# Optimization experiments

Measured on AMD Instinct MI355X. Metric: run time of the kernel, lower is better.

## Reference

```python
import jax, jax.numpy as jnp
import numpy as np
from jax import lax

B, CIN, H, W = 64, 16, 256, 256
COUT, K = 64, 3

def setup_inputs() -> dict:
    key = jax.random.key(0)
    k1, k2, k3 = jax.random.split(key, 3)
    x = jax.random.normal(k1, (B, CIN, H, W), dtype=jnp.float32)
    # PyTorch Conv2d default init scale ~ 1/sqrt(fan_in)
    fan_in = CIN * K * K
    conv_weight = jax.random.normal(k2, (COUT, CIN, K, K), dtype=jnp.float32) / np.sqrt(fan_in)
    conv_bias = jax.random.normal(k3, (COUT,), dtype=jnp.float32) / np.sqrt(fan_in)
    return {"x": x, "conv_weight": conv_weight, "conv_bias": conv_bias}

def reference(x, conv_weight, conv_bias):
    # conv2d, stride=1, padding=0 (VALID), dilation=1, groups=1
    y = lax.conv_general_dilated(
        x, conv_weight,
        window_strides=(1, 1), padding="VALID",
        dimension_numbers=("NCHW", "OIHW", "NCHW"))
    y = y + conv_bias[None, :, None, None]
    # min over channel dim, keepdim
    y = jnp.min(y, axis=1, keepdims=True)  # [B,1,H',W']
    # double tanh
    return jnp.tanh(jnp.tanh(y))
```

## Files before the change

### kernel.cpp

```cpp
#include <hip/hip_runtime.h>
#include <hip/hip_bf16.h>

#define BATCH 64
#define CIN   16
#define H     256
#define W     256
#define HW    (H*W)
#define COUT  64
#define HO    254
#define WO    254

#define TS     16
#define TIN    18
#define CELL   24
#define NTY    8
#define NITEMS (4*TIN*TIN)
#define IPT    6

typedef short  bf16x8 __attribute__((ext_vector_type(8)));
typedef float  f32x16 __attribute__((ext_vector_type(16)));

static __device__ __forceinline__ unsigned short bfbits(float f) {
    __hip_bfloat16 h = __float2bfloat16(f);
    return *(unsigned short*)&h;
}

static __device__ __forceinline__ bf16x8 ld_frag(const ushort* p) {
    union { uint4 u; bf16x8 b; } cv;
    cv.u = *(const uint4*)p;
    return cv.b;
}

static __device__ __forceinline__ float fast_tanh(float x) {
    x = fminf(fmaxf(x, -15.f), 15.f);
    float e = __expf(2.f * x);
    return (e - 1.f) * __builtin_amdgcn_rcpf(e + 1.f);
}

__global__ void repack_w(const float* __restrict__ w, ushort* __restrict__ wpk) {
    int i = blockIdx.x * 256 + threadIdx.x;
    if (i < 9 * COUT * CIN) {
        int ci   = i & 15;
        int cout = (i >> 4) & 63;
        int tap  = i >> 10;
        wpk[i] = bfbits(w[(cout * CIN + ci) * 9 + tap]);
    }
}

__global__ __launch_bounds__(256, 2)
void conv_min_tanh_strip(const float* __restrict__ x,
                         const float* __restrict__ bias,
                         const ushort* __restrict__ wpk,
                         float* __restrict__ out) {
    __shared__ __align__(16) ushort xsm[2][TIN * TIN * CELL];

    const int bid    = blockIdx.x;
    const int L      = (bid & 7) * 256 + (bid >> 3);
    const int b      = L >> 5;
    const int rr     = L & 31;
    const int yb0    = (rr >> 4) * (NTY * TS);
    const int x0     = (rr & 15) * TS;

    const int tid  = threadIdx.x;
    const int lane = tid & 63;
    const int wv   = tid >> 6;
    const int l31  = lane & 31;
    const int hi   = lane >> 5;

    const float* xb0 = x + (size_t)b * (CIN * HW);
    const float* xb1 = xb0 + HW;
    const float* xb2 = xb0 + 2 * HW;
    const float* xb3 = xb0 + 3 * HW;

    bf16x8 wf[9][2];
    #pragma unroll
    for (int tap = 0; tap < 9; ++tap)
        #pragma unroll
        for (int m = 0; m < 2; ++m)
            wf[tap][m] = ld_frag(wpk + tap * 1024 + (m * 32 + l31) * 16 + hi * 8);

    float bini[2][16];
    #pragma unroll
    for (int m = 0; m < 2; ++m)
        #pragma unroll
        for (int r = 0; r < 16; ++r)
            bini[m][r] = bias[m * 32 + (r & 3) + 8 * (r >> 2) + 4 * hi];

    int c0[IPT], dyv[IPT], lo[IPT];
    #pragma unroll
    for (int k = 0; k < IPT; ++k) {
        int it = tid + k * 256;
        int dx = it % TIN;
        int t2 = it / TIN;
        int dy = t2 % TIN;
        int cg = t2 / TIN;
        c0[k]  = cg * 4 * HW + min(x0 + dx, W - 1);
        dyv[k] = dy;
        lo[k]  = (dy * TIN + dx) * CELL + cg * 4;
    }

    const int py_b = wv * 4 + (l31 >> 4);
    const int pxc  = l31 & 15;
    const int cb0  = ((py_b + 0) * TIN + pxc) * CELL + hi * 8;
    const int cb1  = ((py_b + 2) * TIN + pxc) * CELL + hi * 8;

    float fx[IPT][4];

    auto stage_load = [&](int ybase) {
        #pragma unroll
        for (int k = 0; k < IPT; ++k) {
            if (k < 5 || tid < NITEMS - 5 * 256) {
                int gy  = min(ybase + dyv[k], H - 1);
                int idx = c0[k] + (gy << 8);
                fx[k][0] = xb0[idx];
                fx[k][1] = xb1[idx];
                fx[k][2] = xb2[idx];
                fx[k][3] = xb3[idx];
            }
        }
    };
    auto stage_write = [&](int buf) {
        #pragma unroll
        for (int k = 0; k < IPT; ++k) {
            if (k < 5 || tid < NITEMS - 5 * 256) {
                ushort4 v;
                v.x = bfbits(fx[k][0]);
                v.y = bfbits(fx[k][1]);
                v.z = bfbits(fx[k][2]);
                v.w = bfbits(fx[k][3]);
                *(ushort4*)&xsm[buf][lo[k]] = v;
            }
        }
    };

    stage_load(yb0);
    stage_write(0);
    __syncthreads();

    for (int t = 0; t < NTY; ++t) {
        const int cur = t & 1;

        if (t + 1 < NTY) stage_load(yb0 + (t + 1) * TS);

        f32x16 acc[2][2];
        #pragma unroll
        for (int m = 0; m < 2; ++m)
            #pragma unroll
            for (int r = 0; r < 16; ++r) {
                acc[m][0][r] = bini[m][r];
                acc[m][1][r] = bini[m][r];
            }

        const ushort* xt = &xsm[cur][0];
        #pragma unroll
        for (int tap = 0; tap < 9; ++tap) {
            const int kh = tap / 3, kw = tap - 3 * kh;
            const int toff = (kh * TIN + kw) * CELL;
            bf16x8 p0 = ld_frag(xt + cb0 + toff);
            bf16x8 p1 = ld_frag(xt + cb1 + toff);
            acc[0][0] = __builtin_amdgcn_mfma_f32_32x32x16_bf16(wf[tap][0], p0, acc[0][0], 0, 0, 0);
            acc[0][1] = __builtin_amdgcn_mfma_f32_32x32x16_bf16(wf[tap][0], p1, acc[0][1], 0, 0, 0);
            acc[1][0] = __builtin_amdgcn_mfma_f32_32x32x16_bf16(wf[tap][1], p0, acc[1][0], 0, 0, 0);
            acc[1][1] = __builtin_amdgcn_mfma_f32_32x32x16_bf16(wf[tap][1], p1, acc[1][1], 0, 0, 0);
        }

        float res[2];
        #pragma unroll
        for (int n = 0; n < 2; ++n) {
            float v[16];
            #pragma unroll
            for (int r = 0; r < 16; ++r)
                v[r] = fminf(acc[0][n][r], acc[1][n][r]);
            #pragma unroll
            for (int s = 8; s >= 1; s >>= 1)
                #pragma unroll
                for (int r = 0; r < s; ++r)
                    v[r] = fminf(v[r], v[r + s]);
            res[n] = fminf(v[0], __shfl_xor(v[0], 32, 64));
        }
        float val = hi ? res[1] : res[0];
        int px_lin = wv * 64 + lane;
        int oy = yb0 + t * TS + (px_lin >> 4);
        int ox = x0 + (px_lin & 15);
        if (oy < HO && ox < WO)
            out[((size_t)b * HO + oy) * WO + ox] = fast_tanh(fast_tanh(val));

        if (t + 1 < NTY) stage_write(cur ^ 1);
        __syncthreads();
    }
}

extern "C" void kernel_launch(void* const* d_in, const int* in_sizes, int n_in,
                              void* d_out, int out_size, void* d_ws, size_t ws_size,
                              hipStream_t stream) {
    const float* x    = (const float*)d_in[0];
    const float* w    = (const float*)d_in[1];
    const float* bias = (const float*)d_in[2];
    float* out        = (float*)d_out;
    ushort* wpk       = (ushort*)d_ws;

    hipLaunchKernelGGL(repack_w, dim3(36), dim3(256), 0, stream, w, wpk);
    hipLaunchKernelGGL(conv_min_tanh_strip, dim3(2048), dim3(256), 0, stream,
                       x, bias, wpk, out);
}
```

Measured before the change: 106.9 us.

## Deepen input prefetch to two tiles and fold bias into an extra MFMA

Input loading now runs two tiles ahead, ping-ponging between two register sets. This hides more global-load latency behind the MFMA work, and the LDS staging write moves before the epilogue. The bias is packed as a tenth weight tap and multiplied by a constant 'one' fragment, which frees the 32 bias-init registers. The cost is an extra MFMA per accumulator per tile, plus one more bf16 rounding of the bias. The barrier is lowered to a bare lgkmcnt wait plus s_barrier, and MFMA priority is raised with s_setprio. Register pressure rises from the second prefetch buffer and the extra weight fragments.

```diff
diff --git a/kernel.cpp b/kernel.cpp
--- a/kernel.cpp
+++ b/kernel.cpp
@@ -37,29 +37,34 @@
     return (e - 1.f) * __builtin_amdgcn_rcpf(e + 1.f);
 }
 
-__global__ void repack_w(const float* __restrict__ w, ushort* __restrict__ wpk) {
+__global__ void repack_w(const float* __restrict__ w, const float* __restrict__ bias,
+                         ushort* __restrict__ wpk) {
     int i = blockIdx.x * 256 + threadIdx.x;
     if (i < 9 * COUT * CIN) {
         int ci   = i & 15;
         int cout = (i >> 4) & 63;
         int tap  = i >> 10;
         wpk[i] = bfbits(w[(cout * CIN + ci) * 9 + tap]);
+    } else if (i < 10 * COUT * CIN) {
+        int j    = i - 9 * COUT * CIN;
+        int ci   = j & 15;
+        int cout = j >> 4;
+        wpk[i] = (ci == 0) ? bfbits(bias[cout]) : (ushort)0;
     }
 }
 
 __global__ __launch_bounds__(256, 2)
 void conv_min_tanh_strip(const float* __restrict__ x,
-                         const float* __restrict__ bias,
                          const ushort* __restrict__ wpk,
                          float* __restrict__ out) {
     __shared__ __align__(16) ushort xsm[2][TIN * TIN * CELL];
 
-    const int bid    = blockIdx.x;
-    const int L      = (bid & 7) * 256 + (bid >> 3);
-    const int b      = L >> 5;
-    const int rr     = L & 31;
-    const int yb0    = (rr >> 4) * (NTY * TS);
-    const int x0     = (rr & 15) * TS;
+    const int bid = blockIdx.x;
+    const int L   = (bid & 7) * 256 + (bid >> 3);
+    const int b   = L >> 5;
+    const int rr  = L & 31;
+    const int yb0 = (rr >> 4) * (NTY * TS);
+    const int x0  = (rr & 15) * TS;
 
     const int tid  = threadIdx.x;
     const int lane = tid & 63;
@@ -67,24 +72,22 @@
     const int l31  = lane & 31;
     const int hi   = lane >> 5;
 
-    const float* xb0 = x + (size_t)b * (CIN * HW);
-    const float* xb1 = xb0 + HW;
-    const float* xb2 = xb0 + 2 * HW;
-    const float* xb3 = xb0 + 3 * HW;
-
-    bf16x8 wf[9][2];
+    const float* xp0 = x + (size_t)b * (CIN * HW);
+    const float* xp1 = xp0 + HW;
+    const float* xp2 = xp0 + 2 * HW;
+    const float* xp3 = xp0 + 3 * HW;
+
+    bf16x8 wf[10][2];
     #pragma unroll
-    for (int tap = 0; tap < 9; ++tap)
+    for (int tap = 0; tap < 10; ++tap)
         #pragma unroll
         for (int m = 0; m < 2; ++m)
             wf[tap][m] = ld_frag(wpk + tap * 1024 + (m * 32 + l31) * 16 + hi * 8);
 
-    float bini[2][16];
+    bf16x8 pone;
     #pragma unroll
-    for (int m = 0; m < 2; ++m)
-        #pragma unroll
-        for (int r = 0; r < 16; ++r)
-            bini[m][r] = bias[m * 32 + (r & 3) + 8 * (r >> 2) + 4 * hi];
+    for (int j = 0; j < 8; ++j) pone[j] = 0;
+    if (hi == 0) pone[0] = (short)0x3F80;
 
     int c0[IPT], dyv[IPT], lo[IPT];
     #pragma unroll
@@ -104,22 +107,22 @@
     const int cb0  = ((py_b + 0) * TIN + pxc) * CELL + hi * 8;
     const int cb1  = ((py_b + 2) * TIN + pxc) * CELL + hi * 8;
 
-    float fx[IPT][4];
-
-    auto stage_load = [&](int ybase) {
+    float fxA[IPT][4], fxB[IPT][4];
+
+    auto stage_load = [&](int ybase, float (&fx)[IPT][4]) {
         #pragma unroll
         for (int k = 0; k < IPT; ++k) {
             if (k < 5 || tid < NITEMS - 5 * 256) {
                 int gy  = min(ybase + dyv[k], H - 1);
                 int idx = c0[k] + (gy << 8);
-                fx[k][0] = xb0[idx];
-                fx[k][1] = xb1[idx];
-                fx[k][2] = xb2[idx];
-                fx[k][3] = xb3[idx];
+                fx[k][0] = xp0[idx];
+                fx[k][1] = xp1[idx];
+                fx[k][2] = xp2[idx];
+                fx[k][3] = xp3[idx];
             }
         }
     };
-    auto stage_write = [&](int buf) {
+    auto stage_write = [&](int buf, float (&fx)[IPT][4]) {
         #pragma unroll
         for (int k = 0; k < IPT; ++k) {
             if (k < 5 || tid < NITEMS - 5 * 256) {
@@ -133,25 +136,30 @@
         }
     };
 
-    stage_load(yb0);
-    stage_write(0);
-    __syncthreads();
-
-    for (int t = 0; t < NTY; ++t) {
+    auto tile_barrier = [&]() {
+        asm volatile("s_waitcnt lgkmcnt(0)" ::: "memory");
+        __builtin_amdgcn_s_barrier();
+        asm volatile("" ::: "memory");
+    };
+
+    stage_load(yb0, fxA);
+    stage_write(0, fxA);
+    stage_load(yb0 + TS, fxA);
+    tile_barrier();
+
+    auto tile_body = [&](int t, float (&fxw)[IPT][4], float (&fxl)[IPT][4]) {
         const int cur = t & 1;
 
-        if (t + 1 < NTY) stage_load(yb0 + (t + 1) * TS);
+        if (t + 2 < NTY) stage_load(yb0 + (t + 2) * TS, fxl);
 
         f32x16 acc[2][2];
         #pragma unroll
         for (int m = 0; m < 2; ++m)
             #pragma unroll
-            for (int r = 0; r < 16; ++r) {
-                acc[m][0][r] = bini[m][r];
-                acc[m][1][r] = bini[m][r];
-            }
+            for (int r = 0; r < 16; ++r) { acc[m][0][r] = 0.f; acc[m][1][r] = 0.f; }
 
         const ushort* xt = &xsm[cur][0];
+        __builtin_amdgcn_s_setprio(1);
         #pragma unroll
         for (int tap = 0; tap < 9; ++tap) {
             const int kh = tap / 3, kw = tap - 3 * kh;
@@ -163,6 +171,13 @@
             acc[1][0] = __builtin_amdgcn_mfma_f32_32x32x16_bf16(wf[tap][1], p0, acc[1][0], 0, 0, 0);
             acc[1][1] = __builtin_amdgcn_mfma_f32_32x32x16_bf16(wf[tap][1], p1, acc[1][1], 0, 0, 0);
         }
+        acc[0][0] = __builtin_amdgcn_mfma_f32_32x32x16_bf16(wf[9][0], pone, acc[0][0], 0, 0, 0);
+        acc[0][1] = __builtin_amdgcn_mfma_f32_32x32x16_bf16(wf[9][0], pone, acc[0][1], 0, 0, 0);
+        acc[1][0] = __builtin_amdgcn_mfma_f32_32x32x16_bf16(wf[9][1], pone, acc[1][0], 0, 0, 0);
+        acc[1][1] = __builtin_amdgcn_mfma_f32_32x32x16_bf16(wf[9][1], pone, acc[1][1], 0, 0, 0);
+        __builtin_amdgcn_s_setprio(0);
+
+        if (t + 1 < NTY) stage_write(cur ^ 1, fxw);
 
         float res[2];
         #pragma unroll
@@ -185,8 +200,13 @@
         if (oy < HO && ox < WO)
             out[((size_t)b * HO + oy) * WO + ox] = fast_tanh(fast_tanh(val));
 
-        if (t + 1 < NTY) stage_write(cur ^ 1);
-        __syncthreads();
+        tile_barrier();
+    };
+
+    #pragma unroll 1
+    for (int t = 0; t < NTY; t += 2) {
+        tile_body(t,     fxA, fxB);
+        tile_body(t + 1, fxB, fxA);
     }
 }
 
@@ -199,7 +219,7 @@
     float* out        = (float*)d_out;
     ushort* wpk       = (ushort*)d_ws;
 
-    hipLaunchKernelGGL(repack_w, dim3(36), dim3(256), 0, stream, w, wpk);
+    hipLaunchKernelGGL(repack_w, dim3(40), dim3(256), 0, stream, w, bias, wpk);
     hipLaunchKernelGGL(conv_min_tanh_strip, dim3(2048), dim3(256), 0, stream,
-                       x, bias, wpk, out);
-}
+                       x, wpk, out);
+}
```

Result: no change. 108.0 us (+1.0%).
